# Performance work log

Measured on AMD Instinct MI355X. Metric: run time of the kernel, lower is better.

## Reference

```python
import jax, jax.numpy as jnp
import numpy as np

B, T_ENC, T_DEC = 32, 512, 32
ENC = DEC = EMB = ATT = OUT = 256
VOCAB = 32000
CHUNK = 8
SOS = 1


def _energy(enc, h, W, V, b, vv, g, vb, r):
    # enc: [B,T,ENC], h: [B,DEC] -> [B,T]
    t = jnp.tanh(enc @ W.T + (h @ V.T)[:, None, :] + b)           # [B,T,ATT]
    w_eff = (g[0] / jnp.linalg.norm(vv)) * vv                      # weight-normed v
    return t @ w_eff + vb[0] + r[0]


def _excl_cumprod(x):
    # exclusive safe cumprod along axis 1: [1, x0, x0*x1, ...]
    logs = jnp.cumsum(jnp.log(jnp.clip(x, 1e-10, 1.0)), axis=1)
    logs = jnp.concatenate([jnp.zeros_like(logs[:, :1]), logs[:, :-1]], axis=1)
    return jnp.exp(logs)


def _moving_sum(x, back, forward):
    # sliding-window sum over axis 1, window [j-back, j+forward]
    T = x.shape[1]
    w = back + forward + 1
    xp = jnp.pad(x, ((0, 0), (back, forward)))
    c = jnp.cumsum(xp, axis=1)
    c = jnp.concatenate([jnp.zeros_like(c[:, :1]), c], axis=1)
    return c[:, w:w + T] - c[:, :T]


def _chunkwise_beta(alpha, u, w):
    u = u - jnp.max(u, axis=1, keepdims=True)
    eu = jnp.exp(u)
    denom = jnp.clip(_moving_sum(eu, w - 1, 0), 1e-10, None)
    return eu * _moving_sum(alpha / denom, 0, w - 1)


def setup_inputs():
    key = jax.random.key(0)
    ks = jax.random.split(key, 20)
    s = 0.05
    rn = lambda k, shp: jax.random.normal(k, shp, jnp.float32) * s
    return {
        'encoder_outputs': jax.random.normal(ks[0], (B, T_ENC, ENC), jnp.float32),
        'decoder_inputs': jax.random.randint(ks[1], (B, T_DEC), 0, VOCAB),
        'h0': jax.random.normal(ks[2], (B, DEC), jnp.float32),
        'noise': jax.random.normal(ks[3], (T_DEC, B, T_ENC), jnp.float32),
        'emb': rn(ks[4], (VOCAB, EMB)),
        'W_ih': rn(ks[5], (DEC, EMB)), 'b_ih': jnp.zeros((DEC,), jnp.float32),
        'W_hh': rn(ks[6], (DEC, DEC)), 'b_hh': jnp.zeros((DEC,), jnp.float32),
        'Wm': rn(ks[7], (ATT, ENC)), 'Vm': rn(ks[8], (ATT, DEC)),
        'bm': rn(ks[9], (ATT,)), 'vvm': jax.random.normal(ks[10], (ATT,), jnp.float32),
        'gm': jnp.full((1,), (1.0 / ATT) ** 0.5, jnp.float32),
        'vbm': jnp.zeros((1,), jnp.float32), 'rm': jnp.full((1,), -4.0, jnp.float32),
        'Wc': rn(ks[11], (ATT, ENC)), 'Vc': rn(ks[12], (ATT, DEC)),
        'bc': rn(ks[13], (ATT,)), 'vvc': jax.random.normal(ks[14], (ATT,), jnp.float32),
        'gc': jnp.full((1,), (1.0 / ATT) ** 0.5, jnp.float32),
        'vbc': jnp.zeros((1,), jnp.float32), 'rc': jnp.full((1,), -4.0, jnp.float32),
        'W_comb': rn(ks[15], (OUT, ENC + DEC)),
        'W_proj': rn(ks[16], (VOCAB, OUT)), 'b_proj': jnp.zeros((VOCAB,), jnp.float32),
    }


def reference(encoder_outputs, decoder_inputs, h0, noise, emb,
              W_ih, b_ih, W_hh, b_hh,
              Wm, Vm, bm, vvm, gm, vbm, rm,
              Wc, Vc, bc, vvc, gc, vbc, rc,
              W_comb, W_proj, b_proj):
    batch = encoder_outputs.shape[0]
    alpha0 = jnp.zeros((batch, encoder_outputs.shape[1]), encoder_outputs.dtype).at[:, 0].set(1.0)
    x0 = jnp.full((batch,), SOS, dtype=decoder_inputs.dtype)

    def step(carry, xs):
        x_tok, h, alpha = carry
        noise_t, next_tok = xs
        x = emb[x_tok]                                             # embedding lookup
        h = jnp.tanh(x @ W_ih.T + b_ih + h @ W_hh.T + b_hh)        # RNNCell (tanh)
        e_m = _energy(encoder_outputs, h, Wm, Vm, bm, vvm, gm, vbm, rm)
        p = jax.nn.sigmoid(e_m + noise_t)
        cp = _excl_cumprod(1.0 - p)
        alpha = p * cp * jnp.cumsum(alpha / jnp.clip(cp, 1e-10, 1.0), axis=1)
        e_c = _energy(encoder_outputs, h, Wc, Vc, bc, vvc, gc, vbc, rc)
        beta = _chunkwise_beta(alpha, e_c, CHUNK)
        context = jnp.einsum('bt,bte->be', beta, encoder_outputs)
        attn = jnp.tanh(jnp.concatenate([context, h], axis=1) @ W_comb.T)
        logit = attn @ W_proj.T + b_proj
        return (next_tok, h, alpha), logit

    xs = (noise, decoder_inputs.T)
    _, logits = jax.lax.scan(step, (x0, h0, alpha0), xs)           # [T_dec,B,V]
    return jnp.transpose(logits, (1, 0, 2))                        # [B,T_dec,V]
```

## Files before the change

kernel.cpp:

```cpp
#include <hip/hip_runtime.h>
#include <cstddef>

#define B 32
#define T_ENC 512
#define T_DEC 32
#define E 256
#define VOCAB 32000
#define SOS 1
#define NEG2LOG2E -2.885390081777927f

typedef __attribute__((ext_vector_type(8))) short short8;
typedef __attribute__((ext_vector_type(4))) float floatx4;

static const size_t OFF_ENCW   = 0;
static const size_t OFF_WEFFM  = OFF_ENCW + (size_t)B * T_ENC * 2 * E;
static const size_t OFF_WEFFC  = OFF_WEFFM + E;
static const size_t OFF_BSUM   = OFF_WEFFC + E;
static const size_t OFF_XIH    = OFF_BSUM + E;
static const size_t OFF_WHHT   = OFF_XIH + (size_t)T_DEC * B * E;
static const size_t OFF_VMT    = OFF_WHHT + (size_t)E * E;
static const size_t OFF_VCT    = OFF_VMT + (size_t)E * E;
static const size_t OFF_WCOMBT = OFF_VCT + (size_t)E * E;
static const size_t OFF_ATTNB  = OFF_WCOMBT + (size_t)2 * E * E;
static const size_t OFF_WPBF   = OFF_ATTNB + (size_t)T_DEC * B * E / 2;

static const size_t OUT_EMBX  = 0;
static const size_t OUT_BETA  = 262144;
static const size_t OUT_ACOMB = 786432;
static const size_t OUT_HALL  = 1310720;
static const size_t OUT_HV    = 1572864;
static const size_t OUT_PE    = 2097152;
static const size_t OUT_VMC   = 3145728;
static const size_t OUT_ZERO  = 3276800;
static const size_t OUT_WHI   = 3277312;
static const size_t OUT_WLO   = 3342848;
static const size_t OUT_B512  = 3408384;

__device__ __forceinline__ float ftanh(float x) {
  float ax = __builtin_fabsf(x);
  float e  = __expf(-2.f * ax);
  float r  = (1.f - e) * __builtin_amdgcn_rcpf(1.f + e);
  return __builtin_copysignf(r, x);
}

__device__ __forceinline__ float fsigmoid(float z) {
  return __builtin_amdgcn_rcpf(1.f + __expf(-z));
}

__device__ __forceinline__ float wredmax(float s) {
  s = fmaxf(s, __shfl_xor(s, 1, 64));  s = fmaxf(s, __shfl_xor(s, 2, 64));
  s = fmaxf(s, __shfl_xor(s, 4, 64));  s = fmaxf(s, __shfl_xor(s, 8, 64));
  s = fmaxf(s, __shfl_xor(s, 16, 64)); s = fmaxf(s, __shfl_xor(s, 32, 64));
  return s;
}

__device__ __forceinline__ unsigned short f2bf(float f) {
  unsigned int u = __float_as_uint(f);
  u = (u + 0x7fffu + ((u >> 16) & 1u)) >> 16;
  return (unsigned short)u;
}

__device__ __forceinline__ float bf2f(unsigned short h) {
  return __uint_as_float((unsigned int)h << 16);
}

__device__ __forceinline__ float wexcl(float tot, int lane) {
  float v = tot;
#pragma unroll
  for (int off = 1; off < 64; off <<= 1) {
    float y = __shfl_up(v, off, 64);
    if (lane >= off) v += y;
  }
  return v - tot;
}

__device__ __forceinline__ float dot4_wtanh(float4 s2a, float4 s2b, float4 w4) {
  float e, num, acc;
  e = __builtin_exp2f(s2a.x + s2b.x); num = __builtin_fmaf(-e, w4.x, w4.x);
  acc = num * __builtin_amdgcn_rcpf(1.f + e);
  e = __builtin_exp2f(s2a.y + s2b.y); num = __builtin_fmaf(-e, w4.y, w4.y);
  acc = __builtin_fmaf(num, __builtin_amdgcn_rcpf(1.f + e), acc);
  e = __builtin_exp2f(s2a.z + s2b.z); num = __builtin_fmaf(-e, w4.z, w4.z);
  acc = __builtin_fmaf(num, __builtin_amdgcn_rcpf(1.f + e), acc);
  e = __builtin_exp2f(s2a.w + s2b.w); num = __builtin_fmaf(-e, w4.w, w4.w);
  acc = __builtin_fmaf(num, __builtin_amdgcn_rcpf(1.f + e), acc);
  return acc;
}

__device__ __forceinline__ float4 scalem2(float4 v) {
  float4 r;
  r.x = NEG2LOG2E * v.x; r.y = NEG2LOG2E * v.y;
  r.z = NEG2LOG2E * v.z; r.w = NEG2LOG2E * v.w;
  return r;
}

__global__ __launch_bounds__(256) void prep_all(
    const float* __restrict__ vvm, const float* __restrict__ gm, float* __restrict__ w_effm,
    const float* __restrict__ vvc, const float* __restrict__ gc, float* __restrict__ w_effc,
    const float* __restrict__ b_ih, const float* __restrict__ b_hh, float* __restrict__ bsum,
    const float* __restrict__ bm, const float* __restrict__ bc, float* __restrict__ bias512,
    const float* __restrict__ Vm, const float* __restrict__ Vc,
    float* __restrict__ Vmc, float* __restrict__ zero512,
    const float* __restrict__ Wm, const float* __restrict__ Wc,
    unsigned short* __restrict__ Whi, unsigned short* __restrict__ Wlo,
    const float* __restrict__ W_hh, float* __restrict__ W_hhT,
    const float* __restrict__ W_comb, float* __restrict__ W_combT,
    const int* __restrict__ dec, const float* __restrict__ emb, float* __restrict__ embX,
    const float* __restrict__ W_proj, unsigned short* __restrict__ Wp_bf)
{
  __shared__ float red[256];
  __shared__ float tl[32][33];
  const int blk = blockIdx.x, tid = threadIdx.x;
  if (blk < 2) {
    const float* vv = blk ? vvc : vvm;
    const float* g  = blk ? gc  : gm;
    float* out      = blk ? w_effc : w_effm;
    float v = vv[tid];
    red[tid] = v * v;
    __syncthreads();
    for (int off = 128; off > 0; off >>= 1) {
      if (tid < off) red[tid] += red[tid + off];
      __syncthreads();
    }
    float norm = sqrtf(red[0]);
    out[tid] = (g[0] / norm) * v;
  } else if (blk == 2) {
    bsum[tid] = b_ih[tid] + b_hh[tid];
    bias512[tid]       = bm[tid];
    bias512[256 + tid] = bc[tid];
    zero512[tid] = 0.f;
    zero512[256 + tid] = 0.f;
  } else if (blk < 131) {
    int i = (blk - 3) * 1024 + tid * 4;
    float4 v = (i < E * E) ? *(const float4*)(Vm + i) : *(const float4*)(Vc + i - E * E);
    *(float4*)(Vmc + i) = v;
  } else if (blk < 259) {
    int i = (blk - 131) * 1024 + tid * 4;
    float4 v = (i < E * E) ? *(const float4*)(Wm + i) : *(const float4*)(Wc + i - E * E);
    ushort4 h, l;
    h.x = f2bf(v.x); l.x = f2bf(v.x - bf2f(h.x));
    h.y = f2bf(v.y); l.y = f2bf(v.y - bf2f(h.y));
    h.z = f2bf(v.z); l.z = f2bf(v.z - bf2f(h.z));
    h.w = f2bf(v.w); l.w = f2bf(v.w - bf2f(h.w));
    *(ushort4*)(Whi + i) = h;
    *(ushort4*)(Wlo + i) = l;
  } else if (blk < 451) {
    int k2 = blk - 259;
    const float* in; float* out; int C, bx, by;
    if (k2 < 64) { in = W_hh;   out = W_hhT;   C = 256; bx = k2 & 7;  by = k2 >> 3; }
    else { int k = k2 - 64; in = W_comb; out = W_combT; C = 512; bx = k & 15; by = k >> 4; }
    const int R = 256;
    const int tx = tid & 31, ty = tid >> 5;
    const int c0 = bx * 32, r0 = by * 32;
#pragma unroll
    for (int k = 0; k < 4; k++)
      tl[ty + 8 * k][tx] = in[(size_t)(r0 + ty + 8 * k) * C + c0 + tx];
    __syncthreads();
#pragma unroll
    for (int k = 0; k < 4; k++)
      out[(size_t)(c0 + ty + 8 * k) * R + r0 + tx] = tl[tx][ty + 8 * k];
  } else if (blk < 1475) {
    int r = blk - 451;
    int s = r >> 5, b = r & 31;
    int tok = (s == 0) ? SOS : dec[b * T_DEC + s - 1];
    embX[(size_t)r * E + tid] = emb[(size_t)tok * E + tid];
  } else {
    size_t i = ((size_t)(blk - 1475) * 256 + tid) * 4;
    float4 v = *(const float4*)(W_proj + i);
    ushort4 o;
    o.x = f2bf(v.x); o.y = f2bf(v.y); o.z = f2bf(v.z); o.w = f2bf(v.w);
    *(ushort4*)(Wp_bf + i) = o;
  }
}

__global__ __launch_bounds__(256) void gemm_xwt(
    const float* __restrict__ A, const float* __restrict__ W,
    const float* __restrict__ bias, float* __restrict__ Y,
    int M, int N, int K)
{
  __shared__ float As[64][68];
  __shared__ float Ws[64][68];
  const int tid = threadIdx.x;
  const int tx = tid & 15, ty = tid >> 4;
  const int row0 = blockIdx.y * 64, col0 = blockIdx.x * 64;
  float acc[4][4];
#pragma unroll
  for (int i = 0; i < 4; i++)
#pragma unroll
    for (int j = 0; j < 4; j++) acc[i][j] = 0.f;

  for (int k0 = 0; k0 < K; k0 += 64) {
#pragma unroll
    for (int s = 0; s < 4; s++) {
      int i = (s << 4) + ty;
      int j = tx << 2;
      float4 av = *(const float4*)(A + (size_t)(row0 + i) * K + k0 + j);
      As[j][i] = av.x; As[j + 1][i] = av.y; As[j + 2][i] = av.z; As[j + 3][i] = av.w;
      float4 wv = *(const float4*)(W + (size_t)(col0 + i) * K + k0 + j);
      Ws[j][i] = wv.x; Ws[j + 1][i] = wv.y; Ws[j + 2][i] = wv.z; Ws[j + 3][i] = wv.w;
    }
    __syncthreads();
#pragma unroll
    for (int kk = 0; kk < 64; kk++) {
      const float4 af = *(const float4*)&As[kk][ty << 2];
      const float4 bf = *(const float4*)&Ws[kk][tx << 2];
      acc[0][0] += af.x * bf.x; acc[0][1] += af.x * bf.y; acc[0][2] += af.x * bf.z; acc[0][3] += af.x * bf.w;
      acc[1][0] += af.y * bf.x; acc[1][1] += af.y * bf.y; acc[1][2] += af.y * bf.z; acc[1][3] += af.y * bf.w;
      acc[2][0] += af.z * bf.x; acc[2][1] += af.z * bf.y; acc[2][2] += af.z * bf.z; acc[2][3] += af.z * bf.w;
      acc[3][0] += af.w * bf.x; acc[3][1] += af.w * bf.y; acc[3][2] += af.w * bf.z; acc[3][3] += af.w * bf.w;
    }
    __syncthreads();
  }
  const float4 bv = *(const float4*)(bias + col0 + (tx << 2));
#pragma unroll
  for (int i = 0; i < 4; i++) {
    float4 o;
    o.x = acc[i][0] + bv.x; o.y = acc[i][1] + bv.y;
    o.z = acc[i][2] + bv.z; o.w = acc[i][3] + bv.w;
    *(float4*)(Y + (size_t)(row0 + (ty << 2) + i) * N + col0 + (tx << 2)) = o;
  }
}

__global__ __launch_bounds__(1024, 1) void hchain_enc(
    const float* __restrict__ Xih, const float* __restrict__ W_hhT,
    const float* __restrict__ h0,
    float* __restrict__ A_comb, float* __restrict__ h_all,
    const float* __restrict__ encA,
    const unsigned short* __restrict__ Whi, const unsigned short* __restrict__ Wlo,
    const float* __restrict__ bias512, float* __restrict__ encW)
{
  __shared__ __align__(16) unsigned char smem_raw[67584];
  const int tid = threadIdx.x;

  if (blockIdx.x < B) {
    float* h_s = (float*)smem_raw;
    float* red = h_s + 256;
    const int b = blockIdx.x;
    const int c = tid >> 8, d = tid & 255, k0 = c * 64;
    float wreg[64];
#pragma unroll
    for (int j = 0; j < 64; ++j) wreg[j] = W_hhT[(size_t)(k0 + j) * E + d];
    if (tid < E) h_s[tid] = h0[(size_t)b * E + tid];
    __syncthreads();
    for (int s = 0; s < T_DEC; ++s) {
      float acc = 0.f;
#pragma unroll
      for (int j = 0; j < 64; j += 4) {
        float4 hh = *(const float4*)&h_s[k0 + j];
        acc += hh.x * wreg[j] + hh.y * wreg[j + 1] + hh.z * wreg[j + 2] + hh.w * wreg[j + 3];
      }
      red[tid] = acc;
      __syncthreads();
      if (tid < E) {
        float v = red[tid] + red[256 + tid] + red[512 + tid] + red[768 + tid]
                + Xih[((size_t)s * B + b) * E + tid];
        float hh = ftanh(v);
        h_s[tid] = hh;
        A_comb[((size_t)(b * T_DEC + s)) * (2 * E) + E + tid] = hh;
        h_all[((size_t)(b * T_DEC + s)) * E + tid] = hh;
      }
      __syncthreads();
    }
  } else {
    unsigned short* a_hi = (unsigned short*)smem_raw;
    unsigned short* a_lo = a_hi + 64 * 264;
    const int row0 = (int)(blockIdx.x - B) * 64;
#pragma unroll
    for (int u = 0; u < 4; ++u) {
      int f = tid + (u << 10);
      int r = f >> 6, cc = (f & 63) << 2;
      float4 v = *(const float4*)(encA + (size_t)(row0 + r) * E + cc);
      ushort4 h, l;
      h.x = f2bf(v.x); l.x = f2bf(v.x - bf2f(h.x));
      h.y = f2bf(v.y); l.y = f2bf(v.y - bf2f(h.y));
      h.z = f2bf(v.z); l.z = f2bf(v.z - bf2f(h.z));
      h.w = f2bf(v.w); l.w = f2bf(v.w - bf2f(h.w));
      *(ushort4*)&a_hi[r * 264 + cc] = h;
      *(ushort4*)&a_lo[r * 264 + cc] = l;
    }
    __syncthreads();
    const int lane = tid & 63, w = tid >> 6;
    const int m = lane & 15, q = lane >> 4;
    const int c0 = w << 5;
    floatx4 acc[4][2] = {};
    for (int k0 = 0; k0 < E; k0 += 32) {
      const size_t w0 = (size_t)(c0 + m) * E + (q << 3) + k0;
      const size_t w1 = (size_t)(c0 + 16 + m) * E + (q << 3) + k0;
      short8 bh0 = *(const short8*)(Whi + w0);
      short8 bl0 = *(const short8*)(Wlo + w0);
      short8 bh1 = *(const short8*)(Whi + w1);
      short8 bl1 = *(const short8*)(Wlo + w1);
#pragma unroll
      for (int rg = 0; rg < 4; ++rg) {
        short8 ah = *(const short8*)&a_hi[((rg << 4) + m) * 264 + (q << 3) + k0];
        short8 al = *(const short8*)&a_lo[((rg << 4) + m) * 264 + (q << 3) + k0];
        acc[rg][0] = __builtin_amdgcn_mfma_f32_16x16x32_bf16(ah, bh0, acc[rg][0], 0, 0, 0);
        acc[rg][0] = __builtin_amdgcn_mfma_f32_16x16x32_bf16(al, bh0, acc[rg][0], 0, 0, 0);
        acc[rg][0] = __builtin_amdgcn_mfma_f32_16x16x32_bf16(ah, bl0, acc[rg][0], 0, 0, 0);
        acc[rg][0] = __builtin_amdgcn_mfma_f32_16x16x32_bf16(al, bl0, acc[rg][0], 0, 0, 0);
        acc[rg][1] = __builtin_amdgcn_mfma_f32_16x16x32_bf16(ah, bh1, acc[rg][1], 0, 0, 0);
        acc[rg][1] = __builtin_amdgcn_mfma_f32_16x16x32_bf16(al, bh1, acc[rg][1], 0, 0, 0);
        acc[rg][1] = __builtin_amdgcn_mfma_f32_16x16x32_bf16(ah, bl1, acc[rg][1], 0, 0, 0);
        acc[rg][1] = __builtin_amdgcn_mfma_f32_16x16x32_bf16(al, bl1, acc[rg][1], 0, 0, 0);
      }
    }
    const float bia0 = bias512[c0 + m], bia1 = bias512[c0 + 16 + m];
#pragma unroll
    for (int rg = 0; rg < 4; ++rg)
#pragma unroll
      for (int r = 0; r < 4; ++r) {
        const size_t row = row0 + (rg << 4) + (q << 2) + r;
        encW[row * (2 * E) + c0 + m]      = acc[rg][0][r] + bia0;
        encW[row * (2 * E) + c0 + 16 + m] = acc[rg][1][r] + bia1;
      }
  }
}

__global__ __launch_bounds__(512) void energy_kernel(
    const float* __restrict__ encW, const float* __restrict__ g_hv,
    const float* __restrict__ w_effm, const float* __restrict__ w_effc,
    const float* __restrict__ vbm, const float* __restrict__ rmp,
    const float* __restrict__ vbc, const float* __restrict__ rcp_,
    float* __restrict__ g_pe)
{
  __shared__ float hv_s[16 * 512];
  const int b = blockIdx.x, t0 = blockIdx.y << 5, s0 = blockIdx.z << 4;
  const int tid = threadIdx.x, lane = tid & 63, w = tid >> 6;
  const float* hvb = g_hv + ((size_t)(b * T_DEC + s0)) * 512;
  for (int i = tid * 4; i < 16 * 512; i += 2048) {
    float4 v = *(const float4*)(hvb + i);
    *(float4*)&hv_s[i] = scalem2(v);
  }
  __syncthreads();

  const float embias = vbm[0] + rmp[0];
  const float ecbias = vbc[0] + rcp_[0];
  const float bias_l = ((lane >> 2) & 1) ? ecbias : embias;
  const float4 wm4 = *(const float4*)(w_effm + lane * 4);
  const float4 wc4 = *(const float4*)(w_effc + lane * 4);
  const int t = t0 + (w << 2);
  const size_t rb = ((size_t)(b * T_ENC + t)) * 512 + lane * 4;
  const float4 em0 = scalem2(*(const float4*)(encW + rb));
  const float4 em1 = scalem2(*(const float4*)(encW + rb + 512));
  const float4 em2 = scalem2(*(const float4*)(encW + rb + 1024));
  const float4 em3 = scalem2(*(const float4*)(encW + rb + 1536));
  const float4 ec0 = scalem2(*(const float4*)(encW + rb + 256));
  const float4 ec1 = scalem2(*(const float4*)(encW + rb + 768));
  const float4 ec2 = scalem2(*(const float4*)(encW + rb + 1280));
  const float4 ec3 = scalem2(*(const float4*)(encW + rb + 1792));

  const bool sb0 = lane & 1, sb1 = lane & 2, sb2 = lane & 4;
  const int myr = lane >> 3;
  float pv0 = 0.f, pv1 = 0.f;

  for (int sl = 0; sl < 16; ++sl) {
    const float4 hm4 = *(const float4*)&hv_s[(sl << 9) + lane * 4];
    const float4 hc4 = *(const float4*)&hv_s[(sl << 9) + 256 + lane * 4];
    float v0 = dot4_wtanh(em0, hm4, wm4);
    float v1 = dot4_wtanh(em1, hm4, wm4);
    float v2 = dot4_wtanh(em2, hm4, wm4);
    float v3 = dot4_wtanh(em3, hm4, wm4);
    float v4 = dot4_wtanh(ec0, hc4, wc4);
    float v5 = dot4_wtanh(ec1, hc4, wc4);
    float v6 = dot4_wtanh(ec2, hc4, wc4);
    float v7 = dot4_wtanh(ec3, hc4, wc4);
    float k0_ = sb0 ? v1 : v0, s0_ = sb0 ? v0 : v1; k0_ += __shfl_xor(s0_, 1, 64);
    float k1_ = sb0 ? v3 : v2, s1_ = sb0 ? v2 : v3; k1_ += __shfl_xor(s1_, 1, 64);
    float k2_ = sb0 ? v5 : v4, s2_ = sb0 ? v4 : v5; k2_ += __shfl_xor(s2_, 1, 64);
    float k3_ = sb0 ? v7 : v6, s3_ = sb0 ? v6 : v7; k3_ += __shfl_xor(s3_, 1, 64);
    float kA = sb1 ? k1_ : k0_, sA = sb1 ? k0_ : k1_; kA += __shfl_xor(sA, 2, 64);
    float kB = sb1 ? k3_ : k2_, sB = sb1 ? k2_ : k3_; kB += __shfl_xor(sB, 2, 64);
    float dd = sb2 ? kB : kA, sD = sb2 ? kA : kB; dd += __shfl_xor(sD, 4, 64);
    dd += __shfl_xor(dd, 8, 64);
    dd += __shfl_xor(dd, 16, 64);
    dd += __shfl_xor(dd, 32, 64);
    float val = dd + bias_l;
    if ((sl & 7) == myr) {
      if (sl & 8) pv1 = val; else pv0 = val;
    }
  }
  const int row_l = lane & 3, type = (lane >> 2) & 1;
  const int tS = t + row_l;
  const int col = type * 32 + s0 + myr;
  g_pe[((size_t)((b << 6) + col)) * 512 + tS]     = pv0;
  g_pe[((size_t)((b << 6) + col + 8)) * 512 + tS] = pv1;
}

__global__ __launch_bounds__(64) void scan_kernel(
    const float* __restrict__ g_pe, const float* __restrict__ noise,
    float* __restrict__ beta_all)
{
  const int b = blockIdx.x, lane = threadIdx.x;
  const float* pe = g_pe + ((size_t)b << 15);
  float alpha[8];
#pragma unroll
  for (int i = 0; i < 8; ++i) alpha[i] = 0.f;
  if (lane == 0) alpha[0] = 1.f;

  for (int s = 0; s < T_DEC; ++s) {
    const float* nrow = noise + ((size_t)s * B + b) * T_ENC + lane * 8;
    float4 n0 = *(const float4*)nrow;
    float4 n1 = *(const float4*)(nrow + 4);
    float nz[8] = {n0.x, n0.y, n0.z, n0.w, n1.x, n1.y, n1.z, n1.w};
    const float* psm = pe + (size_t)s * 512 + lane * 8;
    const float* pec = pe + (size_t)(32 + s) * 512 + lane * 8;
    float4 m0 = *(const float4*)psm;
    float4 m1 = *(const float4*)(psm + 4);
    float4 e0 = *(const float4*)pec;
    float4 e1 = *(const float4*)(pec + 4);
    float smv[8] = {m0.x, m0.y, m0.z, m0.w, m1.x, m1.y, m1.z, m1.w};
    float ec[8]  = {e0.x, e0.y, e0.z, e0.w, e1.x, e1.y, e1.z, e1.w};
    float p[8];
#pragma unroll
    for (int i = 0; i < 8; ++i) p[i] = fsigmoid(smv[i] + nz[i]);
    float lgv[8], lci[8], run = 0.f;
#pragma unroll
    for (int i = 0; i < 8; ++i) {
      float omp = fminf(fmaxf(1.f - p[i], 1e-10f), 1.f);
      lgv[i] = __logf(omp);
      run += lgv[i];
      lci[i] = run;
    }
    float mloc = ec[0];
#pragma unroll
    for (int i = 1; i < 8; ++i) mloc = fmaxf(mloc, ec[i]);
    float ex1 = wexcl(run, lane);
    float mx  = wredmax(mloc);
    float cp[8], ao[8], eu[8];
#pragma unroll
    for (int i = 0; i < 8; ++i) {
      float incl = lci[i] + ex1;
      cp[i] = __expf(incl - lgv[i]);
      float cpc = fminf(fmaxf(cp[i], 1e-10f), 1.f);
      ao[i] = alpha[i] * __builtin_amdgcn_rcpf(cpc);
      eu[i] = __expf(ec[i] - mx);
    }
    float run2 = 0.f, lc2[8], run3 = 0.f, c1[8];
#pragma unroll
    for (int i = 0; i < 8; ++i) {
      run2 += ao[i]; lc2[i] = run2;
      run3 += eu[i]; c1[i] = run3;
    }
    float ex2 = wexcl(run2, lane);
    float ex3 = wexcl(run3, lane);
    float alpha_new[8];
#pragma unroll
    for (int i = 0; i < 8; ++i) {
      alpha_new[i] = p[i] * cp[i] * (lc2[i] + ex2);
      c1[i] += ex3;
    }
    float r[8];
#pragma unroll
    for (int i = 0; i < 8; ++i) {
      float up = __shfl_up(c1[i], 1, 64);
      float prev = (lane == 0) ? 0.f : up;
      float denom = fmaxf(c1[i] - prev, 1e-10f);
      r[i] = alpha_new[i] * __builtin_amdgcn_rcpf(denom);
    }
    float run4 = 0.f, c2[8];
#pragma unroll
    for (int i = 0; i < 8; ++i) { run4 += r[i]; c2[i] = run4; }
    float ex4 = wexcl(run4, lane);
#pragma unroll
    for (int i = 0; i < 8; ++i) c2[i] += ex4;
    float c2_7 = c2[7];
    float dn[8];
#pragma unroll
    for (int i = 0; i < 8; ++i) dn[i] = __shfl_down(c2[i], 1, 64);
    float up7 = __shfl_up(c2_7, 1, 64);
    float beta[8];
#pragma unroll
    for (int i = 0; i < 8; ++i) {
      float hi = (i == 0) ? c2_7 : ((lane == 63) ? c2_7 : dn[i - 1]);
      float lo = (i == 0) ? ((lane == 0) ? 0.f : up7) : c2[i - 1];
      beta[i] = eu[i] * (hi - lo);
    }
    float* bp = beta_all + ((size_t)(b * T_DEC + s)) * T_ENC + lane * 8;
    *(float4*)bp       = (float4){beta[0], beta[1], beta[2], beta[3]};
    *(float4*)(bp + 4) = (float4){beta[4], beta[5], beta[6], beta[7]};
#pragma unroll
    for (int i = 0; i < 8; ++i) alpha[i] = alpha_new[i];
  }
}

__global__ __launch_bounds__(256) void context_kernel(
    const float* __restrict__ beta_all, const float* __restrict__ enc,
    float* __restrict__ A_comb)
{
  __shared__ float smem[T_ENC * 36];
  const int b = blockIdx.x, e0 = blockIdx.y << 6;
  const int tid = threadIdx.x;
  const float* bp = beta_all + (size_t)b * T_DEC * T_ENC;
  for (int i = tid; i < T_DEC * T_ENC; i += 256) {
    int s2 = i >> 9, t = i & 511;
    smem[t * 36 + s2] = bp[i];
  }
  __syncthreads();
  const int el = tid & 63, tg = tid >> 6;
  float4 a8[8];
#pragma unroll
  for (int u = 0; u < 8; ++u) a8[u] = (float4){0.f, 0.f, 0.f, 0.f};
  const float* ep = enc + (size_t)b * T_ENC * E + e0 + el;
  for (int t = tg; t < T_ENC; t += 4) {
    float v = ep[(size_t)t * E];
    const float4* bt = (const float4*)&smem[t * 36];
#pragma unroll
    for (int u = 0; u < 8; ++u) {
      float4 bv = bt[u];
      a8[u].x += bv.x * v; a8[u].y += bv.y * v;
      a8[u].z += bv.z * v; a8[u].w += bv.w * v;
    }
  }
  __syncthreads();
#pragma unroll
  for (int u = 0; u < 8; ++u) {
    smem[((tg * T_DEC + u * 4 + 0) << 6) + el] = a8[u].x;
    smem[((tg * T_DEC + u * 4 + 1) << 6) + el] = a8[u].y;
    smem[((tg * T_DEC + u * 4 + 2) << 6) + el] = a8[u].z;
    smem[((tg * T_DEC + u * 4 + 3) << 6) + el] = a8[u].w;
  }
  __syncthreads();
  for (int o = tid; o < T_DEC * 64; o += 256) {
    int s2 = o >> 6, e = o & 63;
    float v = smem[(s2 << 6) + e] + smem[((T_DEC + s2) << 6) + e]
            + smem[((2 * T_DEC + s2) << 6) + e] + smem[((3 * T_DEC + s2) << 6) + e];
    A_comb[((size_t)(b * T_DEC + s2)) * (2 * E) + e0 + e] = v;
  }
}

__global__ __launch_bounds__(256) void comb_tanh_kernel(
    const float* __restrict__ A, const float* __restrict__ Wt,
    unsigned short* __restrict__ attn_bf)
{
  __shared__ float As[64][68];
  __shared__ float Ws[64][68];
  const int tid = threadIdx.x, tx = tid & 15, ty = tid >> 4;
  const int row0 = blockIdx.y * 64, col0 = blockIdx.x * 64;
  float acc[4][4];
#pragma unroll
  for (int i = 0; i < 4; i++)
#pragma unroll
    for (int jj = 0; jj < 4; jj++) acc[i][jj] = 0.f;

  for (int k0 = 0; k0 < 2 * E; k0 += 64) {
#pragma unroll
    for (int ss = 0; ss < 4; ss++) {
      int i = (ss << 4) + ty;
      int jj = tx << 2;
      float4 av = *(const float4*)(A + (size_t)(row0 + i) * (2 * E) + k0 + jj);
      As[jj][i] = av.x; As[jj + 1][i] = av.y; As[jj + 2][i] = av.z; As[jj + 3][i] = av.w;
      float4 wv = *(const float4*)(Wt + (size_t)(k0 + i) * E + col0 + jj);
      *(float4*)&Ws[i][jj] = wv;
    }
    __syncthreads();
#pragma unroll
    for (int kk = 0; kk < 64; kk++) {
      const float4 af = *(const float4*)&As[kk][ty << 2];
      const float4 bf = *(const float4*)&Ws[kk][tx << 2];
      acc[0][0] += af.x * bf.x; acc[0][1] += af.x * bf.y; acc[0][2] += af.x * bf.z; acc[0][3] += af.x * bf.w;
      acc[1][0] += af.y * bf.x; acc[1][1] += af.y * bf.y; acc[1][2] += af.y * bf.z; acc[1][3] += af.y * bf.w;
      acc[2][0] += af.z * bf.x; acc[2][1] += af.z * bf.y; acc[2][2] += af.z * bf.z; acc[2][3] += af.z * bf.w;
      acc[3][0] += af.w * bf.x; acc[3][1] += af.w * bf.y; acc[3][2] += af.w * bf.z; acc[3][3] += af.w * bf.w;
    }
    __syncthreads();
  }
#pragma unroll
  for (int i = 0; i < 4; i++) {
    ushort4 o;
    o.x = f2bf(ftanh(acc[i][0])); o.y = f2bf(ftanh(acc[i][1]));
    o.z = f2bf(ftanh(acc[i][2])); o.w = f2bf(ftanh(acc[i][3]));
    *(ushort4*)(attn_bf + (size_t)(row0 + (ty << 2) + i) * E + col0 + (tx << 2)) = o;
  }
}

__global__ __launch_bounds__(256) void proj_mfma(
    const unsigned short* __restrict__ A, const unsigned short* __restrict__ Bw,
    const float* __restrict__ bias, float* __restrict__ Y)
{
  __shared__ unsigned short wl[64][264];
  __shared__ float tile[64][68];
  const int tid = threadIdx.x;
  const int wave = tid >> 6, lane = tid & 63;
  const int m = lane & 15, q = lane >> 4;
  const int col0 = (blockIdx.x >> 1) * 64;
  const int mt0 = (blockIdx.x & 1) * 8;
#pragma unroll
  for (int u = 0; u < 16; ++u) {
    int f = tid + (u << 8);
    int r = f >> 6, c = (f & 63) << 2;
    *(ushort4*)&wl[r][c] = *(const ushort4*)(Bw + (size_t)(col0 + r) * E + c);
  }
  __syncthreads();

  for (int mt = mt0; mt < mt0 + 8; ++mt) {
    const int rowa = mt * 64 + wave * 16;
    floatx4 acc0 = {0.f, 0.f, 0.f, 0.f}, acc1 = acc0, acc2 = acc0, acc3 = acc0;
    const unsigned short* ar = A + (size_t)(rowa + m) * E + q * 8;
#pragma unroll
    for (int k0 = 0; k0 < E; k0 += 32) {
      short8 af = *(const short8*)(ar + k0);
      short8 b0 = *(const short8*)&wl[ 0 + m][q * 8 + k0];
      short8 b1 = *(const short8*)&wl[16 + m][q * 8 + k0];
      short8 b2 = *(const short8*)&wl[32 + m][q * 8 + k0];
      short8 b3 = *(const short8*)&wl[48 + m][q * 8 + k0];
      acc0 = __builtin_amdgcn_mfma_f32_16x16x32_bf16(af, b0, acc0, 0, 0, 0);
      acc1 = __builtin_amdgcn_mfma_f32_16x16x32_bf16(af, b1, acc1, 0, 0, 0);
      acc2 = __builtin_amdgcn_mfma_f32_16x16x32_bf16(af, b2, acc2, 0, 0, 0);
      acc3 = __builtin_amdgcn_mfma_f32_16x16x32_bf16(af, b3, acc3, 0, 0, 0);
    }
    const int rl = wave * 16 + q * 4;
#pragma unroll
    for (int r = 0; r < 4; r++) {
      tile[rl + r][ 0 + m] = acc0[r];
      tile[rl + r][16 + m] = acc1[r];
      tile[rl + r][32 + m] = acc2[r];
      tile[rl + r][48 + m] = acc3[r];
    }
    __syncthreads();
    const int row = tid >> 2, seg = tid & 3;
    const size_t yb = ((size_t)mt * 64 + row) * VOCAB + col0;
#pragma unroll
    for (int u = 0; u < 4; u++) {
      int cc = seg * 16 + u * 4;
      float4 v = *(const float4*)&tile[row][cc];
      float4 bb = *(const float4*)(bias + col0 + cc);
      v.x += bb.x; v.y += bb.y; v.z += bb.z; v.w += bb.w;
      *(float4*)(Y + yb + cc) = v;
    }
    __syncthreads();
  }
}

extern "C" void kernel_launch(void* const* d_in, const int* in_sizes, int n_in,
                              void* d_out, int out_size, void* d_ws, size_t ws_size,
                              hipStream_t stream)
{
  (void)in_sizes; (void)n_in; (void)out_size; (void)ws_size;
  const float* enc    = (const float*)d_in[0];
  const int*   dec    = (const int*)d_in[1];
  const float* h0     = (const float*)d_in[2];
  const float* noise  = (const float*)d_in[3];
  const float* emb    = (const float*)d_in[4];
  const float* W_ih   = (const float*)d_in[5];
  const float* b_ih   = (const float*)d_in[6];
  const float* W_hh   = (const float*)d_in[7];
  const float* b_hh   = (const float*)d_in[8];
  const float* Wm     = (const float*)d_in[9];
  const float* Vm     = (const float*)d_in[10];
  const float* bm     = (const float*)d_in[11];
  const float* vvm    = (const float*)d_in[12];
  const float* gm     = (const float*)d_in[13];
  const float* vbm    = (const float*)d_in[14];
  const float* rmp    = (const float*)d_in[15];
  const float* Wc     = (const float*)d_in[16];
  const float* Vc     = (const float*)d_in[17];
  const float* bc     = (const float*)d_in[18];
  const float* vvc    = (const float*)d_in[19];
  const float* gc     = (const float*)d_in[20];
  const float* vbc    = (const float*)d_in[21];
  const float* rcp_   = (const float*)d_in[22];
  const float* W_comb = (const float*)d_in[23];
  const float* W_proj = (const float*)d_in[24];
  const float* b_proj = (const float*)d_in[25];

  float* ws = (float*)d_ws;
  float* encW    = ws + OFF_ENCW;
  float* w_effm  = ws + OFF_WEFFM;
  float* w_effc  = ws + OFF_WEFFC;
  float* bsum    = ws + OFF_BSUM;
  float* Xih     = ws + OFF_XIH;
  float* W_hhT   = ws + OFF_WHHT;
  float* W_combT = ws + OFF_WCOMBT;
  unsigned short* attn_bf = (unsigned short*)(ws + OFF_ATTNB);
  unsigned short* Wp_bf   = (unsigned short*)(ws + OFF_WPBF);

  float* outF = (float*)d_out;
  float* embX     = outF + OUT_EMBX;
  float* beta_all = outF + OUT_BETA;
  float* A_comb   = outF + OUT_ACOMB;
  float* h_all    = outF + OUT_HALL;
  float* g_hv     = outF + OUT_HV;
  float* g_pe     = outF + OUT_PE;
  float* Vmc      = outF + OUT_VMC;
  float* zero512  = outF + OUT_ZERO;
  unsigned short* Whi = (unsigned short*)(outF + OUT_WHI);
  unsigned short* Wlo = (unsigned short*)(outF + OUT_WLO);
  float* bias512  = outF + OUT_B512;

  prep_all<<<9475, 256, 0, stream>>>(vvm, gm, w_effm, vvc, gc, w_effc,
                                     b_ih, b_hh, bsum, bm, bc, bias512,
                                     Vm, Vc, Vmc, zero512, Wm, Wc, Whi, Wlo,
                                     W_hh, W_hhT, W_comb, W_combT,
                                     dec, emb, embX, W_proj, Wp_bf);
  gemm_xwt<<<dim3(E / 64, (T_DEC * B) / 64), 256, 0, stream>>>(embX, W_ih, bsum, Xih,
                                                               T_DEC * B, E, E);
  hchain_enc<<<B + (B * T_ENC) / 64, 1024, 0, stream>>>(
      Xih, W_hhT, h0, A_comb, h_all, enc, Whi, Wlo, bias512, encW);
  gemm_xwt<<<dim3((2 * E) / 64, (T_DEC * B) / 64), 256, 0, stream>>>(
      h_all, Vmc, zero512, g_hv, T_DEC * B, 2 * E, E);
  energy_kernel<<<dim3(B, 16, 2), 512, 0, stream>>>(
      encW, g_hv, w_effm, w_effc, vbm, rmp, vbc, rcp_, g_pe);
  scan_kernel<<<B, 64, 0, stream>>>(g_pe, noise, beta_all);
  context_kernel<<<dim3(B, 4), 256, 0, stream>>>(beta_all, enc, A_comb);
  comb_tanh_kernel<<<dim3(E / 64, (T_DEC * B) / 64), 256, 0, stream>>>(A_comb, W_combT, attn_bf);
  proj_mfma<<<2 * (VOCAB / 64), 256, 0, stream>>>(attn_bf, Wp_bf, b_proj, outF);
}
```

Baseline: 580.0 us.

## Fuse embedding gather and input GEMM into prep, fold scales, transpose beta layout

Folds the embedding gather and the Xih = emb·W_ihᵀ + bias GEMM into the prep_all launch, which removes one kernel launch and the embX round trip. hchain_enc now loads W_hh rows directly with float4 reads instead of a pre-transposed copy. The −2·log2e scaling moves into the encW and g_hv producers so energy_kernel no longer applies it. The scan writes beta in a [B,T,S] layout, and context_kernel reads it from global memory with 8 t-groups and twice as many blocks. The scattered strided beta stores in the scan and the new GEMM branch inside prep_all could add cost.

```diff
diff --git a/kernel.cpp b/kernel.cpp
--- a/kernel.cpp
+++ b/kernel.cpp
@@ -15,16 +15,11 @@
 static const size_t OFF_ENCW   = 0;
 static const size_t OFF_WEFFM  = OFF_ENCW + (size_t)B * T_ENC * 2 * E;
 static const size_t OFF_WEFFC  = OFF_WEFFM + E;
-static const size_t OFF_BSUM   = OFF_WEFFC + E;
-static const size_t OFF_XIH    = OFF_BSUM + E;
-static const size_t OFF_WHHT   = OFF_XIH + (size_t)T_DEC * B * E;
-static const size_t OFF_VMT    = OFF_WHHT + (size_t)E * E;
-static const size_t OFF_VCT    = OFF_VMT + (size_t)E * E;
-static const size_t OFF_WCOMBT = OFF_VCT + (size_t)E * E;
+static const size_t OFF_XIH    = OFF_WEFFC + E;
+static const size_t OFF_WCOMBT = OFF_XIH + (size_t)T_DEC * B * E;
 static const size_t OFF_ATTNB  = OFF_WCOMBT + (size_t)2 * E * E;
 static const size_t OFF_WPBF   = OFF_ATTNB + (size_t)T_DEC * B * E / 2;
 
-static const size_t OUT_EMBX  = 0;
 static const size_t OUT_BETA  = 262144;
 static const size_t OUT_ACOMB = 786432;
 static const size_t OUT_HALL  = 1310720;
@@ -87,35 +82,76 @@
   return acc;
 }
 
-__device__ __forceinline__ float4 scalem2(float4 v) {
-  float4 r;
-  r.x = NEG2LOG2E * v.x; r.y = NEG2LOG2E * v.y;
-  r.z = NEG2LOG2E * v.z; r.w = NEG2LOG2E * v.w;
-  return r;
-}
-
 __global__ __launch_bounds__(256) void prep_all(
+    const int* __restrict__ dec, const float* __restrict__ emb,
+    const float* __restrict__ W_ih,
+    const float* __restrict__ b_ih, const float* __restrict__ b_hh,
+    float* __restrict__ Xih,
     const float* __restrict__ vvm, const float* __restrict__ gm, float* __restrict__ w_effm,
     const float* __restrict__ vvc, const float* __restrict__ gc, float* __restrict__ w_effc,
-    const float* __restrict__ b_ih, const float* __restrict__ b_hh, float* __restrict__ bsum,
     const float* __restrict__ bm, const float* __restrict__ bc, float* __restrict__ bias512,
     const float* __restrict__ Vm, const float* __restrict__ Vc,
     float* __restrict__ Vmc, float* __restrict__ zero512,
     const float* __restrict__ Wm, const float* __restrict__ Wc,
     unsigned short* __restrict__ Whi, unsigned short* __restrict__ Wlo,
-    const float* __restrict__ W_hh, float* __restrict__ W_hhT,
     const float* __restrict__ W_comb, float* __restrict__ W_combT,
-    const int* __restrict__ dec, const float* __restrict__ emb, float* __restrict__ embX,
     const float* __restrict__ W_proj, unsigned short* __restrict__ Wp_bf)
 {
-  __shared__ float red[256];
+  __shared__ float As[64][68];
+  __shared__ float Ws[64][68];
   __shared__ float tl[32][33];
   const int blk = blockIdx.x, tid = threadIdx.x;
-  if (blk < 2) {
-    const float* vv = blk ? vvc : vvm;
-    const float* g  = blk ? gc  : gm;
-    float* out      = blk ? w_effc : w_effm;
+
+  if (blk < 64) {
+    const int tx = tid & 15, ty = tid >> 4;
+    const int row0 = (blk >> 2) * 64, col0 = (blk & 3) * 64;
+    float acc[4][4];
+#pragma unroll
+    for (int i = 0; i < 4; i++)
+#pragma unroll
+      for (int j = 0; j < 4; j++) acc[i][j] = 0.f;
+    for (int k0 = 0; k0 < E; k0 += 64) {
+#pragma unroll
+      for (int s = 0; s < 4; s++) {
+        int i = (s << 4) + ty;
+        int j = tx << 2;
+        int r = row0 + i;
+        int st = r >> 5, bb = r & 31;
+        int tok = (st == 0) ? SOS : dec[bb * T_DEC + st - 1];
+        float4 av = *(const float4*)(emb + (size_t)tok * E + k0 + j);
+        As[j][i] = av.x; As[j + 1][i] = av.y; As[j + 2][i] = av.z; As[j + 3][i] = av.w;
+        float4 wv = *(const float4*)(W_ih + (size_t)(col0 + i) * E + k0 + j);
+        Ws[j][i] = wv.x; Ws[j + 1][i] = wv.y; Ws[j + 2][i] = wv.z; Ws[j + 3][i] = wv.w;
+      }
+      __syncthreads();
+#pragma unroll
+      for (int kk = 0; kk < 64; kk++) {
+        const float4 af = *(const float4*)&As[kk][ty << 2];
+        const float4 bf = *(const float4*)&Ws[kk][tx << 2];
+        acc[0][0] += af.x * bf.x; acc[0][1] += af.x * bf.y; acc[0][2] += af.x * bf.z; acc[0][3] += af.x * bf.w;
+        acc[1][0] += af.y * bf.x; acc[1][1] += af.y * bf.y; acc[1][2] += af.y * bf.z; acc[1][3] += af.y * bf.w;
+        acc[2][0] += af.z * bf.x; acc[2][1] += af.z * bf.y; acc[2][2] += af.z * bf.z; acc[2][3] += af.z * bf.w;
+        acc[3][0] += af.w * bf.x; acc[3][1] += af.w * bf.y; acc[3][2] += af.w * bf.z; acc[3][3] += af.w * bf.w;
+      }
+      __syncthreads();
+    }
+    float4 b1 = *(const float4*)(b_ih + col0 + (tx << 2));
+    float4 b2 = *(const float4*)(b_hh + col0 + (tx << 2));
+#pragma unroll
+    for (int i = 0; i < 4; i++) {
+      float4 o;
+      o.x = acc[i][0] + b1.x + b2.x; o.y = acc[i][1] + b1.y + b2.y;
+      o.z = acc[i][2] + b1.z + b2.z; o.w = acc[i][3] + b1.w + b2.w;
+      *(float4*)(Xih + (size_t)(row0 + (ty << 2) + i) * E + col0 + (tx << 2)) = o;
+    }
+  } else if (blk < 66) {
+    const int k = blk - 64;
+    const float* vv = k ? vvc : vvm;
+    const float* g  = k ? gc  : gm;
+    float* out      = k ? w_effc : w_effm;
     float v = vv[tid];
+    As[0][0] = 0.f;
+    __shared__ float red[256];
     red[tid] = v * v;
     __syncthreads();
     for (int off = 128; off > 0; off >>= 1) {
@@ -124,18 +160,17 @@
     }
     float norm = sqrtf(red[0]);
     out[tid] = (g[0] / norm) * v;
-  } else if (blk == 2) {
-    bsum[tid] = b_ih[tid] + b_hh[tid];
+  } else if (blk == 66) {
     bias512[tid]       = bm[tid];
     bias512[256 + tid] = bc[tid];
     zero512[tid] = 0.f;
     zero512[256 + tid] = 0.f;
-  } else if (blk < 131) {
-    int i = (blk - 3) * 1024 + tid * 4;
+  } else if (blk < 195) {
+    int i = (blk - 67) * 1024 + tid * 4;
     float4 v = (i < E * E) ? *(const float4*)(Vm + i) : *(const float4*)(Vc + i - E * E);
     *(float4*)(Vmc + i) = v;
-  } else if (blk < 259) {
-    int i = (blk - 131) * 1024 + tid * 4;
+  } else if (blk < 323) {
+    int i = (blk - 195) * 1024 + tid * 4;
     float4 v = (i < E * E) ? *(const float4*)(Wm + i) : *(const float4*)(Wc + i - E * E);
     ushort4 h, l;
     h.x = f2bf(v.x); l.x = f2bf(v.x - bf2f(h.x));
@@ -145,27 +180,19 @@
     *(ushort4*)(Whi + i) = h;
     *(ushort4*)(Wlo + i) = l;
   } else if (blk < 451) {
-    int k2 = blk - 259;
-    const float* in; float* out; int C, bx, by;
-    if (k2 < 64) { in = W_hh;   out = W_hhT;   C = 256; bx = k2 & 7;  by = k2 >> 3; }
-    else { int k = k2 - 64; in = W_comb; out = W_combT; C = 512; bx = k & 15; by = k >> 4; }
-    const int R = 256;
+    int k2 = blk - 323;
+    const int bx = k2 & 15, by = k2 >> 4;
     const int tx = tid & 31, ty = tid >> 5;
     const int c0 = bx * 32, r0 = by * 32;
 #pragma unroll
     for (int k = 0; k < 4; k++)
-      tl[ty + 8 * k][tx] = in[(size_t)(r0 + ty + 8 * k) * C + c0 + tx];
+      tl[ty + 8 * k][tx] = W_comb[(size_t)(r0 + ty + 8 * k) * 512 + c0 + tx];
     __syncthreads();
 #pragma unroll
     for (int k = 0; k < 4; k++)
-      out[(size_t)(c0 + ty + 8 * k) * R + r0 + tx] = tl[tx][ty + 8 * k];
-  } else if (blk < 1475) {
-    int r = blk - 451;
-    int s = r >> 5, b = r & 31;
-    int tok = (s == 0) ? SOS : dec[b * T_DEC + s - 1];
-    embX[(size_t)r * E + tid] = emb[(size_t)tok * E + tid];
+      W_combT[(size_t)(c0 + ty + 8 * k) * 256 + r0 + tx] = tl[tx][ty + 8 * k];
   } else {
-    size_t i = ((size_t)(blk - 1475) * 256 + tid) * 4;
+    size_t i = ((size_t)(blk - 451) * 256 + tid) * 4;
     float4 v = *(const float4*)(W_proj + i);
     ushort4 o;
     o.x = f2bf(v.x); o.y = f2bf(v.y); o.z = f2bf(v.z); o.w = f2bf(v.w);
@@ -176,7 +203,7 @@
 __global__ __launch_bounds__(256) void gemm_xwt(
     const float* __restrict__ A, const float* __restrict__ W,
     const float* __restrict__ bias, float* __restrict__ Y,
-    int M, int N, int K)
+    int M, int N, int K, float alpha)
 {
   __shared__ float As[64][68];
   __shared__ float Ws[64][68];
@@ -215,14 +242,14 @@
 #pragma unroll
   for (int i = 0; i < 4; i++) {
     float4 o;
-    o.x = acc[i][0] + bv.x; o.y = acc[i][1] + bv.y;
-    o.z = acc[i][2] + bv.z; o.w = acc[i][3] + bv.w;
+    o.x = alpha * (acc[i][0] + bv.x); o.y = alpha * (acc[i][1] + bv.y);
+    o.z = alpha * (acc[i][2] + bv.z); o.w = alpha * (acc[i][3] + bv.w);
     *(float4*)(Y + (size_t)(row0 + (ty << 2) + i) * N + col0 + (tx << 2)) = o;
   }
 }
 
 __global__ __launch_bounds__(1024, 1) void hchain_enc(
-    const float* __restrict__ Xih, const float* __restrict__ W_hhT,
+    const float* __restrict__ Xih, const float* __restrict__ W_hh,
     const float* __restrict__ h0,
     float* __restrict__ A_comb, float* __restrict__ h_all,
     const float* __restrict__ encA,
@@ -239,7 +266,10 @@
     const int c = tid >> 8, d = tid & 255, k0 = c * 64;
     float wreg[64];
 #pragma unroll
-    for (int j = 0; j < 64; ++j) wreg[j] = W_hhT[(size_t)(k0 + j) * E + d];
+    for (int j = 0; j < 64; j += 4) {
+      float4 wv = *(const float4*)(W_hh + (size_t)d * E + k0 + j);
+      wreg[j] = wv.x; wreg[j + 1] = wv.y; wreg[j + 2] = wv.z; wreg[j + 3] = wv.w;
+    }
     if (tid < E) h_s[tid] = h0[(size_t)b * E + tid];
     __syncthreads();
     for (int s = 0; s < T_DEC; ++s) {
@@ -310,8 +340,8 @@
 #pragma unroll
       for (int r = 0; r < 4; ++r) {
         const size_t row = row0 + (rg << 4) + (q << 2) + r;
-        encW[row * (2 * E) + c0 + m]      = acc[rg][0][r] + bia0;
-        encW[row * (2 * E) + c0 + 16 + m] = acc[rg][1][r] + bia1;
+        encW[row * (2 * E) + c0 + m]      = NEG2LOG2E * (acc[rg][0][r] + bia0);
+        encW[row * (2 * E) + c0 + 16 + m] = NEG2LOG2E * (acc[rg][1][r] + bia1);
       }
   }
 }
@@ -327,10 +357,8 @@
   const int b = blockIdx.x, t0 = blockIdx.y << 5, s0 = blockIdx.z << 4;
   const int tid = threadIdx.x, lane = tid & 63, w = tid >> 6;
   const float* hvb = g_hv + ((size_t)(b * T_DEC + s0)) * 512;
-  for (int i = tid * 4; i < 16 * 512; i += 2048) {
-    float4 v = *(const float4*)(hvb + i);
-    *(float4*)&hv_s[i] = scalem2(v);
-  }
+  for (int i = tid * 4; i < 16 * 512; i += 2048)
+    *(float4*)&hv_s[i] = *(const float4*)(hvb + i);
   __syncthreads();
 
   const float embias = vbm[0] + rmp[0];
@@ -340,14 +368,14 @@
   const float4 wc4 = *(const float4*)(w_effc + lane * 4);
   const int t = t0 + (w << 2);
   const size_t rb = ((size_t)(b * T_ENC + t)) * 512 + lane * 4;
-  const float4 em0 = scalem2(*(const float4*)(encW + rb));
-  const float4 em1 = scalem2(*(const float4*)(encW + rb + 512));
-  const float4 em2 = scalem2(*(const float4*)(encW + rb + 1024));
-  const float4 em3 = scalem2(*(const float4*)(encW + rb + 1536));
-  const float4 ec0 = scalem2(*(const float4*)(encW + rb + 256));
-  const float4 ec1 = scalem2(*(const float4*)(encW + rb + 768));
-  const float4 ec2 = scalem2(*(const float4*)(encW + rb + 1280));
-  const float4 ec3 = scalem2(*(const float4*)(encW + rb + 1792));
+  const float4 em0 = *(const float4*)(encW + rb);
+  const float4 em1 = *(const float4*)(encW + rb + 512);
+  const float4 em2 = *(const float4*)(encW + rb + 1024);
+  const float4 em3 = *(const float4*)(encW + rb + 1536);
+  const float4 ec0 = *(const float4*)(encW + rb + 256);
+  const float4 ec1 = *(const float4*)(encW + rb + 768);
+  const float4 ec2 = *(const float4*)(encW + rb + 1280);
+  const float4 ec3 = *(const float4*)(encW + rb + 1792);
 
   const bool sb0 = lane & 1, sb1 = lane & 2, sb2 = lane & 4;
   const int myr = lane >> 3;
@@ -388,7 +416,7 @@
 
 __global__ __launch_bounds__(64) void scan_kernel(
     const float* __restrict__ g_pe, const float* __restrict__ noise,
-    float* __restrict__ beta_all)
+    float* __restrict__ beta_T)
 {
   const int b = blockIdx.x, lane = threadIdx.x;
   const float* pe = g_pe + ((size_t)b << 15);
@@ -468,42 +496,34 @@
 #pragma unroll
     for (int i = 0; i < 8; ++i) dn[i] = __shfl_down(c2[i], 1, 64);
     float up7 = __shfl_up(c2_7, 1, 64);
-    float beta[8];
 #pragma unroll
     for (int i = 0; i < 8; ++i) {
       float hi = (i == 0) ? c2_7 : ((lane == 63) ? c2_7 : dn[i - 1]);
       float lo = (i == 0) ? ((lane == 0) ? 0.f : up7) : c2[i - 1];
-      beta[i] = eu[i] * (hi - lo);
-    }
-    float* bp = beta_all + ((size_t)(b * T_DEC + s)) * T_ENC + lane * 8;
-    *(float4*)bp       = (float4){beta[0], beta[1], beta[2], beta[3]};
-    *(float4*)(bp + 4) = (float4){beta[4], beta[5], beta[6], beta[7]};
+      float beta = eu[i] * (hi - lo);
+      beta_T[((size_t)(b * T_ENC) + lane * 8 + i) * T_DEC + s] = beta;
+    }
 #pragma unroll
     for (int i = 0; i < 8; ++i) alpha[i] = alpha_new[i];
   }
 }
 
 __global__ __launch_bounds__(256) void context_kernel(
-    const float* __restrict__ beta_all, const float* __restrict__ enc,
+    const float* __restrict__ beta_T, const float* __restrict__ enc,
     float* __restrict__ A_comb)
 {
-  __shared__ float smem[T_ENC * 36];
-  const int b = blockIdx.x, e0 = blockIdx.y << 6;
+  __shared__ float smem[8 * 32 * 33];
+  const int b = blockIdx.x, e0 = blockIdx.y << 5;
   const int tid = threadIdx.x;
-  const float* bp = beta_all + (size_t)b * T_DEC * T_ENC;
-  for (int i = tid; i < T_DEC * T_ENC; i += 256) {
-    int s2 = i >> 9, t = i & 511;
-    smem[t * 36 + s2] = bp[i];
-  }
-  __syncthreads();
-  const int el = tid & 63, tg = tid >> 6;
+  const int el = tid & 31, tg = tid >> 5;
   float4 a8[8];
 #pragma unroll
   for (int u = 0; u < 8; ++u) a8[u] = (float4){0.f, 0.f, 0.f, 0.f};
   const float* ep = enc + (size_t)b * T_ENC * E + e0 + el;
-  for (int t = tg; t < T_ENC; t += 4) {
+  const float* bt0 = beta_T + (size_t)b * T_ENC * T_DEC;
+  for (int t = tg; t < T_ENC; t += 8) {
     float v = ep[(size_t)t * E];
-    const float4* bt = (const float4*)&smem[t * 36];
+    const float4* bt = (const float4*)(bt0 + (size_t)t * T_DEC);
 #pragma unroll
     for (int u = 0; u < 8; ++u) {
       float4 bv = bt[u];
@@ -511,20 +531,16 @@
       a8[u].z += bv.z * v; a8[u].w += bv.w * v;
     }
   }
+  float* my = &smem[(tg * 32 + el) * 33];
+#pragma unroll
+  for (int u = 0; u < 8; ++u) *(float4*)(my + u * 4) = a8[u];
   __syncthreads();
-#pragma unroll
-  for (int u = 0; u < 8; ++u) {
-    smem[((tg * T_DEC + u * 4 + 0) << 6) + el] = a8[u].x;
-    smem[((tg * T_DEC + u * 4 + 1) << 6) + el] = a8[u].y;
-    smem[((tg * T_DEC + u * 4 + 2) << 6) + el] = a8[u].z;
-    smem[((tg * T_DEC + u * 4 + 3) << 6) + el] = a8[u].w;
-  }
-  __syncthreads();
-  for (int o = tid; o < T_DEC * 64; o += 256) {
-    int s2 = o >> 6, e = o & 63;
-    float v = smem[(s2 << 6) + e] + smem[((T_DEC + s2) << 6) + e]
-            + smem[((2 * T_DEC + s2) << 6) + e] + smem[((3 * T_DEC + s2) << 6) + e];
-    A_comb[((size_t)(b * T_DEC + s2)) * (2 * E) + e0 + e] = v;
+  for (int o = tid; o < 32 * 32; o += 256) {
+    int e = o >> 5, s = o & 31;
+    float v = 0.f;
+#pragma unroll
+    for (int g = 0; g < 8; ++g) v += smem[(g * 32 + e) * 33 + s];
+    A_comb[((size_t)(b * T_DEC + s)) * (2 * E) + e0 + e] = v;
   }
 }
 
@@ -667,16 +683,13 @@
   float* encW    = ws + OFF_ENCW;
   float* w_effm  = ws + OFF_WEFFM;
   float* w_effc  = ws + OFF_WEFFC;
-  float* bsum    = ws + OFF_BSUM;
   float* Xih     = ws + OFF_XIH;
-  float* W_hhT   = ws + OFF_WHHT;
   float* W_combT = ws + OFF_WCOMBT;
   unsigned short* attn_bf = (unsigned short*)(ws + OFF_ATTNB);
   unsigned short* Wp_bf   = (unsigned short*)(ws + OFF_WPBF);
 
   float* outF = (float*)d_out;
-  float* embX     = outF + OUT_EMBX;
-  float* beta_all = outF + OUT_BETA;
+  float* beta_T   = outF + OUT_BETA;
   float* A_comb   = outF + OUT_ACOMB;
   float* h_all    = outF + OUT_HALL;
   float* g_hv     = outF + OUT_HV;
@@ -687,21 +700,19 @@
   unsigned short* Wlo = (unsigned short*)(outF + OUT_WLO);
   float* bias512  = outF + OUT_B512;
 
-  prep_all<<<9475, 256, 0, stream>>>(vvm, gm, w_effm, vvc, gc, w_effc,
-                                     b_ih, b_hh, bsum, bm, bc, bias512,
-                                     Vm, Vc, Vmc, zero512, Wm, Wc, Whi, Wlo,
-                                     W_hh, W_hhT, W_comb, W_combT,
-                                     dec, emb, embX, W_proj, Wp_bf);
-  gemm_xwt<<<dim3(E / 64, (T_DEC * B) / 64), 256, 0, stream>>>(embX, W_ih, bsum, Xih,
-                                                               T_DEC * B, E, E);
+  prep_all<<<8451, 256, 0, stream>>>(dec, emb, W_ih, b_ih, b_hh, Xih,
+                                     vvm, gm, w_effm, vvc, gc, w_effc,
+                                     bm, bc, bias512, Vm, Vc, Vmc, zero512,
+                                     Wm, Wc, Whi, Wlo, W_comb, W_combT,
+                                     W_proj, Wp_bf);
   hchain_enc<<<B + (B * T_ENC) / 64, 1024, 0, stream>>>(
-      Xih, W_hhT, h0, A_comb, h_all, enc, Whi, Wlo, bias512, encW);
+      Xih, W_hh, h0, A_comb, h_all, enc, Whi, Wlo, bias512, encW);
   gemm_xwt<<<dim3((2 * E) / 64, (T_DEC * B) / 64), 256, 0, stream>>>(
-      h_all, Vmc, zero512, g_hv, T_DEC * B, 2 * E, E);
+      h_all, Vmc, zero512, g_hv, T_DEC * B, 2 * E, E, NEG2LOG2E);
   energy_kernel<<<dim3(B, 16, 2), 512, 0, stream>>>(
       encW, g_hv, w_effm, w_effc, vbm, rmp, vbc, rcp_, g_pe);
-  scan_kernel<<<B, 64, 0, stream>>>(g_pe, noise, beta_all);
-  context_kernel<<<dim3(B, 4), 256, 0, stream>>>(beta_all, enc, A_comb);
+  scan_kernel<<<B, 64, 0, stream>>>(g_pe, noise, beta_T);
+  context_kernel<<<dim3(B, 8), 256, 0, stream>>>(beta_T, enc, A_comb);
   comb_tanh_kernel<<<dim3(E / 64, (T_DEC * B) / 64), 256, 0, stream>>>(A_comb, W_combT, attn_bf);
   proj_mfma<<<2 * (VOCAB / 64), 256, 0, stream>>>(attn_bf, Wp_bf, b_proj, outF);
 }
```

After: 581.2 us. About the same (+0.2%).
